# Kernel tuning notes

Measured on AMD Instinct MI355X. Metric: run time of the kernel, lower is better.

Reference implementation:

```python
import jax, jax.numpy as jnp
import numpy as np

# Frozen random draws from the original module's sampling ranges
R = 4          # radius in [3, 5]
SIGMA = 1.2    # sigma in [0.8, 1.6]
N_POINTS = 6   # num_points in [5, 7]


def _gauss1d(k, s):
    x = jnp.arange(k, dtype=jnp.float32) - (k - 1) / 2
    g = jnp.exp(-(x * x) / (2 * s * s))
    return g / jnp.maximum(g.sum(), 1e-12)


def setup_inputs() -> dict:
    key = jax.random.key(0)
    k1, k2 = jax.random.split(key)
    d = h = w = 256
    volume = jax.random.normal(k1, (1, d, h, w), dtype=jnp.float32)  # [C=1,d,h,w]
    points = jax.random.randint(k2, (N_POINTS, 3), 0, d)             # (z,y,x) centers
    return {"volume": volume, "points": points}


def reference(volume, points):
    d, h, w = volume.shape[1:]
    k = 2 * R + 1
    g = _gauss1d(k, SIGMA).astype(volume.dtype)
    # full (non-separable) 3D kernel, as in the original F.conv3d call
    ker = (g[:, None, None] * g[None, :, None] * g[None, None, :])[None, None]  # [1,1,k,k,k]
    x = volume[None]  # [1,1,d,h,w]
    blurred = jax.lax.conv_general_dilated(
        x, ker, window_strides=(1, 1, 1), padding=[(R, R)] * 3,
        dimension_numbers=("NCDHW", "OIDHW", "NCDHW"))  # zero-padded, same as padding=r
    # Union of (2R+1)^3 boxes around each point, clipped at volume borders.
    # |coord - p| <= R is exactly the clipped slice region[z0:z1, y0:y1, x0:x1] = True.
    zz, yy, xx = jnp.arange(d), jnp.arange(h), jnp.arange(w)
    region = jnp.zeros((d, h, w), dtype=bool)
    for i in range(points.shape[0]):  # small fixed n (<=7)
        pz, py, px = points[i, 0], points[i, 1], points[i, 2]
        m = ((jnp.abs(zz - pz) <= R)[:, None, None]
             & (jnp.abs(yy - py) <= R)[None, :, None]
             & (jnp.abs(xx - px) <= R)[None, None, :])
        region = region | m
    out = jnp.where(region[None], blurred[0], volume)  # [1,d,h,w]
    return out
```

## Files before the change

### kernel.cpp

```cpp
#include <hip/hip_runtime.h>

#define RAD   4
#define KS    9
#define HALO  8
#define SS    17
#define DIM   256
#define SIG   1.2f

__global__ __launch_bounds__(256) void copy_vol_kernel(
    const float4* __restrict__ in, float4* __restrict__ out, int n4) {
    int stride = gridDim.x * blockDim.x;
    for (int i = blockIdx.x * blockDim.x + threadIdx.x; i < n4; i += stride) {
        out[i] = in[i];
    }
}

__global__ __launch_bounds__(256) void blur_fix_kernel(
    const float* __restrict__ vol, const int* __restrict__ pts,
    float* __restrict__ out) {
    __shared__ float sm[SS * SS * SS];
    __shared__ float t1[KS * SS * SS];
    __shared__ float t2[KS * KS * SS];

    const int p  = blockIdx.x;
    const int tid = threadIdx.x;
    const int pz = pts[3 * p + 0];
    const int py = pts[3 * p + 1];
    const int px = pts[3 * p + 2];

    float g[KS];
    {
        float s = 0.f;
        #pragma unroll
        for (int i = 0; i < KS; ++i) {
            float x = (float)(i - RAD);
            g[i] = expf(-(x * x) / (2.f * SIG * SIG));
            s += g[i];
        }
        float inv = 1.f / s;
        #pragma unroll
        for (int i = 0; i < KS; ++i) g[i] *= inv;
    }

    for (int idx = tid; idx < SS * SS * SS; idx += 256) {
        int k = idx % SS;
        int j = (idx / SS) % SS;
        int i = idx / (SS * SS);
        int z = pz - HALO + i;
        int y = py - HALO + j;
        int x = px - HALO + k;
        float v = 0.f;
        if ((unsigned)z < (unsigned)DIM && (unsigned)y < (unsigned)DIM &&
            (unsigned)x < (unsigned)DIM) {
            v = vol[((z * DIM) + y) * DIM + x];
        }
        sm[idx] = v;
    }
    __syncthreads();

    for (int idx = tid; idx < KS * SS * SS; idx += 256) {
        int k = idx % SS;
        int j = (idx / SS) % SS;
        int i = idx / (SS * SS);
        float acc = 0.f;
        #pragma unroll
        for (int t = 0; t < KS; ++t)
            acc += g[t] * sm[(((i + t) * SS) + j) * SS + k];
        t1[idx] = acc;
    }
    __syncthreads();

    for (int idx = tid; idx < KS * KS * SS; idx += 256) {
        int k = idx % SS;
        int j = (idx / SS) % KS;
        int i = idx / (SS * KS);
        float acc = 0.f;
        #pragma unroll
        for (int t = 0; t < KS; ++t)
            acc += g[t] * t1[((i * SS) + (j + t)) * SS + k];
        t2[((i * KS) + j) * SS + k] = acc;
    }
    __syncthreads();

    for (int idx = tid; idx < KS * KS * KS; idx += 256) {
        int k = idx % KS;
        int j = (idx / KS) % KS;
        int i = idx / (KS * KS);
        float acc = 0.f;
        #pragma unroll
        for (int t = 0; t < KS; ++t)
            acc += g[t] * t2[((i * KS) + j) * SS + (k + t)];
        int z = pz - RAD + i;
        int y = py - RAD + j;
        int x = px - RAD + k;
        if ((unsigned)z < (unsigned)DIM && (unsigned)y < (unsigned)DIM &&
            (unsigned)x < (unsigned)DIM) {
            out[((z * DIM) + y) * DIM + x] = acc;
        }
    }
}

extern "C" void kernel_launch(void* const* d_in, const int* in_sizes, int n_in,
                              void* d_out, int out_size, void* d_ws, size_t ws_size,
                              hipStream_t stream) {
    const float* vol = (const float*)d_in[0];
    const int*   pts = (const int*)d_in[1];
    float*       out = (float*)d_out;

    const int n   = in_sizes[0];
    const int n4  = n / 4;
    const int npt = in_sizes[1] / 3;

    copy_vol_kernel<<<2048, 256, 0, stream>>>(
        (const float4*)vol, (float4*)out, n4);
    blur_fix_kernel<<<npt, 256, 0, stream>>>(vol, pts, out);
}
```

Before: 125.4 us.

## Fuse volume copy and blur into one launch with region-masked copy

Merges the copy kernel and the per-point blur kernel into a single launch. The first NPT blocks compute the blurred boxes, and the remaining blocks copy chunks of the volume while skipping elements inside any point's box, so the two kinds of writes never overlap and no ordering is needed. Copy blocks now each handle a fixed 8-iteration chunk instead of grid-striding. The blur LDS buffers are aliased to cut shared memory, and the point count is made a template parameter. This saves one kernel launch and the serialization between the two kernels, at the cost of per-element region checks in chunks that touch a box.

```diff
diff --git a/kernel.cpp b/kernel.cpp
--- a/kernel.cpp
+++ b/kernel.cpp
@@ -6,98 +6,170 @@
 #define SS    17
 #define DIM   256
 #define SIG   1.2f
+#define IT    8
+#define CHUNK (256 * IT)
 
-__global__ __launch_bounds__(256) void copy_vol_kernel(
-    const float4* __restrict__ in, float4* __restrict__ out, int n4) {
-    int stride = gridDim.x * blockDim.x;
-    for (int i = blockIdx.x * blockDim.x + threadIdx.x; i < n4; i += stride) {
-        out[i] = in[i];
+template <int NPT>
+__global__ __launch_bounds__(256) void fused_kernel(
+    const float* __restrict__ vol, const int* __restrict__ pts,
+    float* __restrict__ out, int n4) {
+
+    __shared__ float lds[SS * SS * SS + KS * SS * SS];
+
+    const int tid = threadIdx.x;
+
+    if ((int)blockIdx.x < NPT) {
+        float* sm = lds;
+        float* t1 = lds + SS * SS * SS;
+        float* t2 = lds;
+
+        const int p  = blockIdx.x;
+        const int pz = pts[3 * p + 0];
+        const int py = pts[3 * p + 1];
+        const int px = pts[3 * p + 2];
+
+        float g[KS];
+        {
+            float s = 0.f;
+            #pragma unroll
+            for (int i = 0; i < KS; ++i) {
+                float x = (float)(i - RAD);
+                g[i] = expf(-(x * x) / (2.f * SIG * SIG));
+                s += g[i];
+            }
+            float inv = 1.f / s;
+            #pragma unroll
+            for (int i = 0; i < KS; ++i) g[i] *= inv;
+        }
+
+        for (int idx = tid; idx < SS * SS * SS; idx += 256) {
+            int k = idx % SS;
+            int j = (idx / SS) % SS;
+            int i = idx / (SS * SS);
+            int z = pz - HALO + i;
+            int y = py - HALO + j;
+            int x = px - HALO + k;
+            float v = 0.f;
+            if ((unsigned)z < (unsigned)DIM && (unsigned)y < (unsigned)DIM &&
+                (unsigned)x < (unsigned)DIM) {
+                v = vol[(z << 16) + (y << 8) + x];
+            }
+            sm[idx] = v;
+        }
+        __syncthreads();
+
+        for (int idx = tid; idx < KS * SS * SS; idx += 256) {
+            int k = idx % SS;
+            int j = (idx / SS) % SS;
+            int i = idx / (SS * SS);
+            float acc = 0.f;
+            #pragma unroll
+            for (int t = 0; t < KS; ++t)
+                acc += g[t] * sm[(((i + t) * SS) + j) * SS + k];
+            t1[idx] = acc;
+        }
+        __syncthreads();
+
+        for (int idx = tid; idx < KS * KS * SS; idx += 256) {
+            int k = idx % SS;
+            int j = (idx / SS) % KS;
+            int i = idx / (SS * KS);
+            float acc = 0.f;
+            #pragma unroll
+            for (int t = 0; t < KS; ++t)
+                acc += g[t] * t1[((i * SS) + (j + t)) * SS + k];
+            t2[((i * KS) + j) * SS + k] = acc;
+        }
+        __syncthreads();
+
+        for (int idx = tid; idx < KS * KS * KS; idx += 256) {
+            int k = idx % KS;
+            int j = (idx / KS) % KS;
+            int i = idx / (KS * KS);
+            float acc = 0.f;
+            #pragma unroll
+            for (int t = 0; t < KS; ++t)
+                acc += g[t] * t2[((i * KS) + j) * SS + (k + t)];
+            int z = pz - RAD + i;
+            int y = py - RAD + j;
+            int x = px - RAD + k;
+            if ((unsigned)z < (unsigned)DIM && (unsigned)y < (unsigned)DIM &&
+                (unsigned)x < (unsigned)DIM) {
+                out[(z << 16) + (y << 8) + x] = acc;
+            }
+        }
+        return;
+    }
+
+    const int c    = blockIdx.x - NPT;
+    const int base = c * CHUNK;
+    const int zb   = base >> 14;
+    const int y0   = (base & 16383) >> 6;
+
+    int pzr[NPT], pyr[NPT], pxr[NPT];
+    #pragma unroll
+    for (int p = 0; p < NPT; ++p) {
+        pzr[p] = pts[3 * p + 0];
+        pyr[p] = pts[3 * p + 1];
+        pxr[p] = pts[3 * p + 2];
+    }
+
+    bool hit = false;
+    #pragma unroll
+    for (int p = 0; p < NPT; ++p)
+        hit |= (abs(zb - pzr[p]) <= RAD) & (pyr[p] + RAD >= y0) &
+               (pyr[p] - RAD <= y0 + 31);
+
+    const float4* __restrict__ in4  = (const float4*)vol;
+    float4* __restrict__       out4 = (float4*)out;
+
+    const bool full = (base + CHUNK <= n4);
+
+    if (!hit && full) {
+        #pragma unroll
+        for (int it = 0; it < IT; ++it) {
+            const int i4 = base + it * 256 + tid;
+            out4[i4] = in4[i4];
+        }
+    } else {
+        for (int it = 0; it < IT; ++it) {
+            const int i4 = base + it * 256 + tid;
+            if (i4 >= n4) break;
+            const float4 v = in4[i4];
+            const int lin = i4 << 2;
+            const int x0  = lin & (DIM - 1);
+            const int y   = (lin >> 8) & (DIM - 1);
+            const int z   = lin >> 16;
+            bool h4 = false;
+            #pragma unroll
+            for (int p = 0; p < NPT; ++p)
+                h4 |= (abs(z - pzr[p]) <= RAD) & (abs(y - pyr[p]) <= RAD) &
+                      (x0 <= pxr[p] + RAD) & (x0 + 3 >= pxr[p] - RAD);
+            if (!h4) {
+                out4[i4] = v;
+            } else {
+                const float r[4] = {v.x, v.y, v.z, v.w};
+                #pragma unroll
+                for (int e = 0; e < 4; ++e) {
+                    const int x = x0 + e;
+                    bool ins = false;
+                    #pragma unroll
+                    for (int p = 0; p < NPT; ++p)
+                        ins |= (abs(z - pzr[p]) <= RAD) &
+                               (abs(y - pyr[p]) <= RAD) &
+                               (abs(x - pxr[p]) <= RAD);
+                    if (!ins) out[lin + e] = r[e];
+                }
+            }
+        }
     }
 }
 
-__global__ __launch_bounds__(256) void blur_fix_kernel(
-    const float* __restrict__ vol, const int* __restrict__ pts,
-    float* __restrict__ out) {
-    __shared__ float sm[SS * SS * SS];
-    __shared__ float t1[KS * SS * SS];
-    __shared__ float t2[KS * KS * SS];
-
-    const int p  = blockIdx.x;
-    const int tid = threadIdx.x;
-    const int pz = pts[3 * p + 0];
-    const int py = pts[3 * p + 1];
-    const int px = pts[3 * p + 2];
-
-    float g[KS];
-    {
-        float s = 0.f;
-        #pragma unroll
-        for (int i = 0; i < KS; ++i) {
-            float x = (float)(i - RAD);
-            g[i] = expf(-(x * x) / (2.f * SIG * SIG));
-            s += g[i];
-        }
-        float inv = 1.f / s;
-        #pragma unroll
-        for (int i = 0; i < KS; ++i) g[i] *= inv;
-    }
-
-    for (int idx = tid; idx < SS * SS * SS; idx += 256) {
-        int k = idx % SS;
-        int j = (idx / SS) % SS;
-        int i = idx / (SS * SS);
-        int z = pz - HALO + i;
-        int y = py - HALO + j;
-        int x = px - HALO + k;
-        float v = 0.f;
-        if ((unsigned)z < (unsigned)DIM && (unsigned)y < (unsigned)DIM &&
-            (unsigned)x < (unsigned)DIM) {
-            v = vol[((z * DIM) + y) * DIM + x];
-        }
-        sm[idx] = v;
-    }
-    __syncthreads();
-
-    for (int idx = tid; idx < KS * SS * SS; idx += 256) {
-        int k = idx % SS;
-        int j = (idx / SS) % SS;
-        int i = idx / (SS * SS);
-        float acc = 0.f;
-        #pragma unroll
-        for (int t = 0; t < KS; ++t)
-            acc += g[t] * sm[(((i + t) * SS) + j) * SS + k];
-        t1[idx] = acc;
-    }
-    __syncthreads();
-
-    for (int idx = tid; idx < KS * KS * SS; idx += 256) {
-        int k = idx % SS;
-        int j = (idx / SS) % KS;
-        int i = idx / (SS * KS);
-        float acc = 0.f;
-        #pragma unroll
-        for (int t = 0; t < KS; ++t)
-            acc += g[t] * t1[((i * SS) + (j + t)) * SS + k];
-        t2[((i * KS) + j) * SS + k] = acc;
-    }
-    __syncthreads();
-
-    for (int idx = tid; idx < KS * KS * KS; idx += 256) {
-        int k = idx % KS;
-        int j = (idx / KS) % KS;
-        int i = idx / (KS * KS);
-        float acc = 0.f;
-        #pragma unroll
-        for (int t = 0; t < KS; ++t)
-            acc += g[t] * t2[((i * KS) + j) * SS + (k + t)];
-        int z = pz - RAD + i;
-        int y = py - RAD + j;
-        int x = px - RAD + k;
-        if ((unsigned)z < (unsigned)DIM && (unsigned)y < (unsigned)DIM &&
-            (unsigned)x < (unsigned)DIM) {
-            out[((z * DIM) + y) * DIM + x] = acc;
-        }
-    }
+template <int NPT>
+static void launch_fused(const float* vol, const int* pts, float* out,
+                         int n4, hipStream_t stream) {
+    const int nCopyBlk = (n4 + CHUNK - 1) / CHUNK;
+    fused_kernel<NPT><<<NPT + nCopyBlk, 256, 0, stream>>>(vol, pts, out, n4);
 }
 
 extern "C" void kernel_launch(void* const* d_in, const int* in_sizes, int n_in,
@@ -111,7 +183,13 @@
     const int n4  = n / 4;
     const int npt = in_sizes[1] / 3;
 
-    copy_vol_kernel<<<2048, 256, 0, stream>>>(
-        (const float4*)vol, (float4*)out, n4);
-    blur_fix_kernel<<<npt, 256, 0, stream>>>(vol, pts, out);
+    switch (npt) {
+        case 1: launch_fused<1>(vol, pts, out, n4, stream); break;
+        case 2: launch_fused<2>(vol, pts, out, n4, stream); break;
+        case 3: launch_fused<3>(vol, pts, out, n4, stream); break;
+        case 4: launch_fused<4>(vol, pts, out, n4, stream); break;
+        case 5: launch_fused<5>(vol, pts, out, n4, stream); break;
+        case 6: launch_fused<6>(vol, pts, out, n4, stream); break;
+        default: launch_fused<7>(vol, pts, out, n4, stream); break;
+    }
 }
```

New measurement: 117.6 us, median of 2. -6.2%, faster.
